# Kernel optimization log

Hardware: AMD Instinct MI355X
Metric: run time of the kernel (lower is better)

Reference implementation:

```python
import jax, jax.numpy as jnp
import numpy as np
from jax import lax

ALPHA = 2.0   # snntorch surrogate.atan(alpha=2.0)
THR = 1.0     # snntorch Leaky default threshold
NUM_STEPS = 8

@jax.custom_vjp
def spike(x):
    # Heaviside forward, ATan surrogate backward (matches snntorch surrogate.atan)
    return (x > 0).astype(x.dtype)

def _spk_fwd(x):
    return (x > 0).astype(x.dtype), x

def _spk_bwd(x, g):
    return (g * (ALPHA / 2.0) / (1.0 + (jnp.pi / 2.0 * ALPHA * x) ** 2),)

spike.defvjp(_spk_fwd, _spk_bwd)


def setup_inputs() -> dict:
    key = jax.random.key(0)
    ks = jax.random.split(key, 7)
    B, D, H, A = 16384, 512, 2048, 8
    H2 = H // 2
    s1 = 1.0 / np.sqrt(D)
    s2 = 1.0 / np.sqrt(H)
    s3 = 1.0 / np.sqrt(H2)
    return {
        "x": jax.random.normal(ks[0], (B, D), jnp.float32),
        "W1": jax.random.uniform(ks[1], (H, D), jnp.float32, -s1, s1),
        "b1": jax.random.uniform(ks[2], (H,), jnp.float32, -s1, s1),
        "W2": jax.random.uniform(ks[3], (H2, H), jnp.float32, -s2, s2),
        "b2": jax.random.uniform(ks[4], (H2,), jnp.float32, -s2, s2),
        "Wo": jax.random.uniform(ks[5], (A, H2), jnp.float32, -s3, s3),
        "bo": jax.random.uniform(ks[6], (A,), jnp.float32, -s3, s3),
        "beta1": jnp.float32(0.9),
        "beta2": jnp.float32(0.85),
        "beta_out": jnp.float32(0.95),
    }


def reference(x, W1, b1, W2, b2, Wo, bo, beta1, beta2, beta_out):
    B = x.shape[0]
    H, H2, A = W1.shape[0], W2.shape[0], Wo.shape[0]
    # snntorch clamps learnable beta into [0, 1] inside the state function
    be1 = jnp.clip(beta1, 0.0, 1.0)
    be2 = jnp.clip(beta2, 0.0, 1.0)
    beo = jnp.clip(beta_out, 0.0, 1.0)

    cur1 = x @ W1.T + b1  # fc1(x) is identical every step; hoist out of the loop

    mem1 = jnp.zeros((B, H), x.dtype)
    mem2 = jnp.zeros((B, H2), x.dtype)
    mem_out = jnp.zeros((B, A), x.dtype)
    max_mem = jnp.full((B, A), -1e9, x.dtype)

    def step(carry, _):
        mem1, mem2, mem_out, max_mem = carry
        # lif1: subtract-reset Leaky; reset uses detached spike of previous mem
        reset1 = lax.stop_gradient(spike(mem1 - THR))
        mem1 = be1 * mem1 + cur1 - reset1 * THR
        spk1 = spike(mem1 - THR)
        # lif2
        reset2 = lax.stop_gradient(spike(mem2 - THR))
        mem2 = be2 * mem2 + (spk1 @ W2.T + b2) - reset2 * THR
        spk2 = spike(mem2 - THR)
        # li_out: reset_mechanism='none' -> pure leaky integrator
        mem_out = beo * mem_out + (spk2 @ Wo.T + bo)
        max_mem = jnp.maximum(max_mem, mem_out)
        return (mem1, mem2, mem_out, max_mem), None

    (mem1, mem2, mem_out, max_mem), _ = lax.scan(
        step, (mem1, mem2, mem_out, max_mem), None, length=NUM_STEPS
    )
    return max_mem
```

## Files before the change

kernel.cpp:

```cpp
#include <hip/hip_runtime.h>
#include <stdint.h>


typedef __bf16 bf16;
typedef __attribute__((ext_vector_type(8))) __bf16 bf16x8;
typedef __attribute__((ext_vector_type(4))) float f32x4;

#define CAP1 2097152
#define CAP2 2097152
#define MARGIN 2e-3f
#define MARGIN2 5e-4f

__device__ __forceinline__ void gl16(const void* g, void* l) {
  __builtin_amdgcn_global_load_lds(
      (const __attribute__((address_space(1))) uint32_t*)g,
      (__attribute__((address_space(3))) uint32_t*)l, 16, 0, 0);
}

__device__ __forceinline__ float clampf(float v) {
  return fminf(fmaxf(v, 0.f), 1.f);
}

__device__ __forceinline__ uint32_t expand2(uint32_t b) {
  return ((b & 1u) ? 0x3F80u : 0u) | ((b & 2u) ? 0x3F800000u : 0u);
}


__global__ void split_x_kernel(const float* __restrict__ x, bf16* __restrict__ Ax) {
  int i = blockIdx.x * 256 + threadIdx.x;
  int b = i >> 9, d = i & 511;
  float v = x[i];
  bf16 hi = (bf16)v;
  bf16 lo = (bf16)(v - (float)hi);
  size_t base = (size_t)b * 1024;
  Ax[base + d] = hi;
  Ax[base + 512 + d] = lo;
}

__global__ void split_w1_kernel(const float* __restrict__ W1, bf16* __restrict__ B0,
                                bf16* __restrict__ B1) {
  int i = blockIdx.x * 256 + threadIdx.x;
  int r = i >> 9, d = i & 511;
  float v = W1[i];
  bf16 hi = (bf16)v;
  bf16 lo = (bf16)(v - (float)hi);
  size_t base = (size_t)r * 1024;
  B0[base + d] = hi;  B0[base + 512 + d] = lo;
  B1[base + d] = lo;  B1[base + 512 + d] = hi;
}

__global__ void split_w2_kernel(const float* __restrict__ W2, bf16* __restrict__ Wh,
                                bf16* __restrict__ Wl) {
  int i = blockIdx.x * 256 + threadIdx.x;
  float v = W2[i];
  bf16 hi = (bf16)v;
  Wh[i] = hi;
  Wl[i] = (bf16)(v - (float)hi);
}


#define SA_OFF  0
#define SB0_OFF 16384
#define SB1_OFF 32768

__global__ __launch_bounds__(256, 2) void gemm1_lif1_kernel(
    const bf16* __restrict__ A, const bf16* __restrict__ B0,
    const bf16* __restrict__ B1, const float* __restrict__ bias,
    const float* __restrict__ beta1p,
    uint32_t* __restrict__ spkbits1, uint2* __restrict__ flag1,
    uint32_t* __restrict__ cnt1)
{
  __shared__ __align__(16) uint8_t lds[49152];
  const int tid = threadIdx.x;
  const int lane = tid & 63;
  const int wave = tid >> 6;
  const int wm = (wave >> 1) * 64, wn = (wave & 1) * 64;
  const size_t brow = (size_t)blockIdx.x * 128;
  const size_t bcol = (size_t)blockIdx.y * 128;
  const int K = 1024;
  const float be = clampf(beta1p[0]);

  const bf16* gA  = A  + brow * K;
  const bf16* gB0 = B0 + bcol * K;
  const bf16* gB1 = B1 + bcol * K;

  f32x4 acc[4][4] = {};

  for (int kk = 0; kk < K; kk += 64) {
#pragma unroll
    for (int q = 0; q < 4; ++q) {
      const int flat = q * 256 + tid;
      const int row = flat >> 3;
      const int s   = flat & 7;
      const int c8  = (s ^ (row & 7)) * 8;
      gl16(gA  + (size_t)row * K + kk + c8, lds + SA_OFF  + flat * 16);
      gl16(gB0 + (size_t)row * K + kk + c8, lds + SB0_OFF + flat * 16);
      gl16(gB1 + (size_t)row * K + kk + c8, lds + SB1_OFF + flat * 16);
    }
    asm volatile("s_waitcnt vmcnt(0)" ::: "memory");
    __syncthreads();
#pragma unroll
    for (int ks = 0; ks < 2; ++ks) {
      bf16x8 af[4], b0f[4], b1f[4];
#pragma unroll
      for (int i = 0; i < 4; ++i) {
        const int ra = wm + i * 16 + (lane & 15);
        const int sa = ((ks * 4 + (lane >> 4)) ^ (ra & 7)) * 16;
        af[i]  = *(const bf16x8*)(lds + SA_OFF  + ra * 128 + sa);
        const int rb = wn + i * 16 + (lane & 15);
        const int sb = ((ks * 4 + (lane >> 4)) ^ (rb & 7)) * 16;
        b0f[i] = *(const bf16x8*)(lds + SB0_OFF + rb * 128 + sb);
        b1f[i] = *(const bf16x8*)(lds + SB1_OFF + rb * 128 + sb);
      }
#pragma unroll
      for (int m = 0; m < 4; ++m)
#pragma unroll
        for (int n = 0; n < 4; ++n) {
          acc[m][n] = __builtin_amdgcn_mfma_f32_16x16x32_bf16(af[m], b0f[n], acc[m][n], 0, 0, 0);
          acc[m][n] = __builtin_amdgcn_mfma_f32_16x16x32_bf16(af[m], b1f[n], acc[m][n], 0, 0, 0);
        }
    }
    __syncthreads();
  }

  uint32_t* lcnt  = (uint32_t*)lds;
  uint32_t* lbase = (uint32_t*)(lds + 4);
  uint2*    llist = (uint2*)(lds + 16);
  const uint32_t CAPL = 3000;
  if (tid == 0) *lcnt = 0;
  __syncthreads();

  const int rg = lane >> 4;
  const bool writer = (lane & 15) == 0;
  uint16_t* sp16 = (uint16_t*)spkbits1;

#pragma unroll
  for (int m = 0; m < 4; ++m)
#pragma unroll
    for (int n = 0; n < 4; ++n) {
      const int chb = (int)(bcol) + wn + n * 16;
      const int w32 = chb >> 5, half = (chb >> 4) & 1;
      const float bv = bias[chb + (lane & 15)];
#pragma unroll
      for (int j = 0; j < 4; ++j) {
        const float c = acc[m][n][j] + bv;
        float mem = 0.f; uint32_t hist = 0; bool nearThr = false;
#pragma unroll
        for (int t = 0; t < 8; ++t) {
          float rst = (mem > 1.f) ? 1.f : 0.f;
          mem = be * mem + c - rst;
          uint32_t bit = (mem > 1.f) ? 1u : 0u;
          hist |= bit << t;
          nearThr |= (fabsf(mem - 1.f) < MARGIN);
        }
#pragma unroll
        for (int t = 0; t < 8; ++t) {
          unsigned long long bal = __ballot((hist >> t) & 1u);
          if (writer) {
            uint32_t row = (uint32_t)(brow + wm + m * 16 + rg * 4 + j);
            size_t idx = ((size_t)(t * 64 + w32) * 16384 + row) * 2 + half;
            sp16[idx] = (uint16_t)(bal >> (rg * 16));
          }
        }
        if (nearThr) {
          const uint32_t h = (uint32_t)(chb + (lane & 15));
          const uint32_t b = (uint32_t)(brow + wm + m * 16 + rg * 4 + j);
          uint2 en; en.x = (h << 14) | b; en.y = hist;
          uint32_t pos = atomicAdd(lcnt, 1u);
          if (pos < CAPL) llist[pos] = en;
          else { uint32_t g = atomicAdd(cnt1, 1u); if (g < CAP1) flag1[g] = en; }
        }
      }
    }

  __syncthreads();
  uint32_t ln = *lcnt; if (ln > CAPL) ln = CAPL;
  if (tid == 0) *lbase = atomicAdd(cnt1, ln);
  __syncthreads();
  const uint32_t gb = *lbase;
  for (uint32_t i = tid; i < ln; i += 256) {
    uint32_t g = gb + i;
    if (g < CAP1) flag1[g] = llist[i];
  }
}


__global__ __launch_bounds__(256) void repair1_kernel(
    const float* __restrict__ x, const float* __restrict__ W1,
    const float* __restrict__ b1, const float* __restrict__ beta1p,
    const uint2* __restrict__ flag1, const uint32_t* __restrict__ cnt1,
    uint32_t* __restrict__ spkbits1)
{
  uint32_t n = cnt1[0]; if (n > CAP1) n = CAP1;
  const float be = clampf(beta1p[0]);
  for (uint32_t i = blockIdx.x * 256 + threadIdx.x; i < n; i += gridDim.x * 256) {
    uint2 e = flag1[i];
    int h = e.x >> 14, b = e.x & 16383;
    const float* xr = x + (size_t)b * 512;
    const float* wr = W1 + (size_t)h * 512;
    float s = 0.f;
    for (int d = 0; d < 512; ++d) s = fmaf(xr[d], wr[d], s);
    s = __fadd_rn(s, b1[h]);
    float m = 0.f; uint32_t eb = 0;
#pragma unroll
    for (int t = 0; t < 8; ++t) {
      float rst = (__fsub_rn(m, 1.f) > 0.f) ? 1.f : 0.f;
      m = __fsub_rn(__fadd_rn(__fmul_rn(be, m), s), rst);
      if (__fsub_rn(m, 1.f) > 0.f) eb |= 1u << t;
    }
    uint32_t diff = eb ^ (e.y & 0xFFu);
    if (diff) {
#pragma unroll
      for (int t = 0; t < 8; ++t)
        if ((diff >> t) & 1u)
          atomicXor(&spkbits1[((size_t)t * 64 + (h >> 5)) * 16384 + b], 1u << (h & 31));
    }
  }
}


__global__ __launch_bounds__(256, 2) void step2_kernel(
    const uint32_t* __restrict__ spkbits1,
    const bf16* __restrict__ W2h, const bf16* __restrict__ W2l,
    const float* __restrict__ b2, const float* __restrict__ beta2p,
    uint32_t* __restrict__ spkbits2, uint32_t* __restrict__ flag2,
    uint32_t* __restrict__ cnt2)
{
  __shared__ __align__(16) uint8_t lds[49152];
  const int K = 2048;
  const int tid = threadIdx.x;
  const int lane = tid & 63;
  const int wave = tid >> 6;
  const int wm = (wave >> 1) * 64, wn = (wave & 1) * 64;
  const size_t brow = (size_t)blockIdx.x * 128;
  const size_t bcol = (size_t)blockIdx.y * 128;
  const float be2 = clampf(beta2p[0]);

  const bf16* gB0 = W2h + bcol * K;
  const bf16* gB1 = W2l + bcol * K;

  float b2c[4];
#pragma unroll
  for (int n = 0; n < 4; ++n) b2c[n] = b2[bcol + wn + n * 16 + (lane & 15)];

  const int ar = tid & 127;
  const int aw = tid >> 7;
  const int rg = lane >> 4;
  const bool writer = (lane & 15) == 0;
  uint16_t* sp16 = (uint16_t*)spkbits2;

  f32x4 acc[4][4] = {};
  unsigned long long flg = 0;

  for (int t = 0; t < 8; ++t) {
#pragma unroll
    for (int m = 0; m < 4; ++m)
#pragma unroll
      for (int n = 0; n < 4; ++n)
#pragma unroll
        for (int j = 0; j < 4; ++j) {
          float v = acc[m][n][j];
          float rst = (v > 1.f) ? 1.f : 0.f;
          acc[m][n][j] = be2 * v + (b2c[n] - rst);
        }

    for (int kk = 0; kk < K; kk += 64) {
      uint32_t bits = spkbits1[((size_t)t * 64 + (kk >> 5) + aw) * 16384 + brow + ar];
#pragma unroll
      for (int c = 0; c < 4; ++c) {
        uint4 u;
        u.x = expand2(bits >> (8 * c));
        u.y = expand2(bits >> (8 * c + 2));
        u.z = expand2(bits >> (8 * c + 4));
        u.w = expand2(bits >> (8 * c + 6));
        const int slot = (aw * 4 + c) ^ (ar & 7);
        *(uint4*)(lds + SA_OFF + ar * 128 + slot * 16) = u;
      }
#pragma unroll
      for (int q = 0; q < 4; ++q) {
        const int flat = q * 256 + tid;
        const int row = flat >> 3;
        const int s   = flat & 7;
        const int c8  = (s ^ (row & 7)) * 8;
        gl16(gB0 + (size_t)row * K + kk + c8, lds + SB0_OFF + flat * 16);
        gl16(gB1 + (size_t)row * K + kk + c8, lds + SB1_OFF + flat * 16);
      }
      asm volatile("s_waitcnt vmcnt(0)" ::: "memory");
      __syncthreads();
#pragma unroll
      for (int ks = 0; ks < 2; ++ks) {
        bf16x8 af[4], b0f[4], b1f[4];
#pragma unroll
        for (int i = 0; i < 4; ++i) {
          const int ra = wm + i * 16 + (lane & 15);
          const int sa = ((ks * 4 + (lane >> 4)) ^ (ra & 7)) * 16;
          af[i] = *(const bf16x8*)(lds + SA_OFF + ra * 128 + sa);
          const int rb = wn + i * 16 + (lane & 15);
          const int sb = ((ks * 4 + (lane >> 4)) ^ (rb & 7)) * 16;
          b0f[i] = *(const bf16x8*)(lds + SB0_OFF + rb * 128 + sb);
          b1f[i] = *(const bf16x8*)(lds + SB1_OFF + rb * 128 + sb);
        }
#pragma unroll
        for (int m = 0; m < 4; ++m)
#pragma unroll
          for (int n = 0; n < 4; ++n) {
            acc[m][n] = __builtin_amdgcn_mfma_f32_16x16x32_bf16(af[m], b0f[n], acc[m][n], 0, 0, 0);
            acc[m][n] = __builtin_amdgcn_mfma_f32_16x16x32_bf16(af[m], b1f[n], acc[m][n], 0, 0, 0);
          }
      }
      __syncthreads();
    }

#pragma unroll
    for (int m = 0; m < 4; ++m)
#pragma unroll
      for (int n = 0; n < 4; ++n) {
        const int chb = (int)(bcol) + wn + n * 16;
        const int w32 = chb >> 5, half = (chb >> 4) & 1;
#pragma unroll
        for (int j = 0; j < 4; ++j) {
          float v = acc[m][n][j];
          if (fabsf(v - 1.f) < MARGIN2) flg |= 1ull << (m * 16 + n * 4 + j);
          unsigned long long bal = __ballot(v > 1.f);
          if (writer) {
            uint32_t row = (uint32_t)(brow + wm + m * 16 + rg * 4 + j);
            size_t idx = ((size_t)(t * 32 + w32) * 16384 + row) * 2 + half;
            sp16[idx] = (uint16_t)(bal >> (rg * 16));
          }
        }
      }
  }

  uint32_t* lcnt  = (uint32_t*)lds;
  uint32_t* lbase = (uint32_t*)(lds + 4);
  uint32_t* llist = (uint32_t*)(lds + 16);
  const uint32_t CAPL = 6000;
  if (tid == 0) *lcnt = 0;
  __syncthreads();

  if (flg) {
#pragma unroll
    for (int m = 0; m < 4; ++m)
#pragma unroll
      for (int n = 0; n < 4; ++n)
#pragma unroll
        for (int j = 0; j < 4; ++j)
          if ((flg >> (m * 16 + n * 4 + j)) & 1ull) {
            const int row = wm + m * 16 + rg * 4 + j;
            const int col = wn + n * 16 + (lane & 15);
            uint32_t en = (uint32_t)(((brow + row) << 10) | (bcol + col));
            uint32_t pos = atomicAdd(lcnt, 1u);
            if (pos < CAPL) llist[pos] = en;
            else { uint32_t g = atomicAdd(cnt2, 1u); if (g < CAP2) flag2[g] = en; }
          }
  }

  __syncthreads();
  uint32_t ln = *lcnt; if (ln > CAPL) ln = CAPL;
  if (tid == 0) *lbase = atomicAdd(cnt2, ln);
  __syncthreads();
  const uint32_t gb = *lbase;
  for (uint32_t i = tid; i < ln; i += 256) {
    uint32_t g = gb + i;
    if (g < CAP2) flag2[g] = llist[i];
  }
}


__global__ __launch_bounds__(256) void repair2_kernel(
    const uint32_t* __restrict__ spkbits1, const float* __restrict__ W2,
    const float* __restrict__ b2, const float* __restrict__ beta2p,
    const uint32_t* __restrict__ flag2, const uint32_t* __restrict__ cnt2,
    uint32_t* __restrict__ spkbits2)
{
  uint32_t n = cnt2[0]; if (n > CAP2) n = CAP2;
  const float be = clampf(beta2p[0]);
  for (uint32_t i = blockIdx.x * 256 + threadIdx.x; i < n; i += gridDim.x * 256) {
    uint32_t e = flag2[i];
    int b = e >> 10, h2 = e & 1023;
    const float* wr = W2 + (size_t)h2 * 2048;
    const float bias = b2[h2];
    float s[8] = {0, 0, 0, 0, 0, 0, 0, 0};
    for (int w = 0; w < 64; ++w) {
      uint32_t bt[8];
#pragma unroll
      for (int t = 0; t < 8; ++t)
        bt[t] = spkbits1[((size_t)t * 64 + w) * 16384 + b];
#pragma unroll 8
      for (int k = 0; k < 32; ++k) {
        const float wv = wr[w * 32 + k];
#pragma unroll
        for (int t = 0; t < 8; ++t) {
          float addend = ((bt[t] >> k) & 1u) ? wv : 0.0f;
          s[t] = __fadd_rn(s[t], addend);
        }
      }
    }
    float m = 0.f;
#pragma unroll
    for (int t = 0; t < 8; ++t) {
      float st = __fadd_rn(s[t], bias);
      float rst = (__fsub_rn(m, 1.f) > 0.f) ? 1.f : 0.f;
      m = __fsub_rn(__fadd_rn(__fmul_rn(be, m), st), rst);
      uint32_t exact = (__fsub_rn(m, 1.f) > 0.f) ? 1u : 0u;
      uint32_t* wp = &spkbits2[((size_t)t * 32 + (h2 >> 5)) * 16384 + b];
      uint32_t stored = (*wp >> (h2 & 31)) & 1u;
      if (stored != exact) atomicXor(wp, 1u << (h2 & 31));
    }
  }
}


__global__ __launch_bounds__(256) void out_kernel(
    const uint32_t* __restrict__ spkbits2, const float* __restrict__ Wo,
    const float* __restrict__ bo, const float* __restrict__ betaop,
    float* __restrict__ out)
{
  const int wave = threadIdx.x >> 6, lane = threadIdx.x & 63;
  const int b = blockIdx.x * 4 + wave;
  const float beo = clampf(betaop[0]);
  const int a = lane & 7;
  const int slice = lane >> 3;

  float s[8] = {0, 0, 0, 0, 0, 0, 0, 0};
#pragma unroll
  for (int q = 0; q < 4; ++q) {
    const int wrd = slice * 4 + q;
    uint32_t wt[8];
#pragma unroll
    for (int t = 0; t < 8; ++t)
      wt[t] = spkbits2[((size_t)(t * 32 + wrd)) * 16384 + b];
    const float* wop = Wo + (size_t)a * 1024 + wrd * 32;
#pragma unroll
    for (int k8 = 0; k8 < 8; ++k8) {
      const float4 wv = *(const float4*)(wop + k8 * 4);
      const float wa[4] = {wv.x, wv.y, wv.z, wv.w};
#pragma unroll
      for (int kk = 0; kk < 4; ++kk) {
        const int k = k8 * 4 + kk;
#pragma unroll
        for (int t = 0; t < 8; ++t)
          s[t] += ((wt[t] >> k) & 1u) ? wa[kk] : 0.0f;
      }
    }
  }
#pragma unroll
  for (int t = 0; t < 8; ++t) {
    s[t] += __shfl_down(s[t], 8, 64);
    s[t] += __shfl_down(s[t], 16, 64);
    s[t] += __shfl_down(s[t], 32, 64);
  }
  if (lane < 8) {
    const float bov = bo[a];
    float mo = 0.f, mx = -1e30f;
#pragma unroll
    for (int t = 0; t < 8; ++t) {
      mo = beo * mo + (s[t] + bov);
      mx = fmaxf(mx, mo);
    }
    out[(size_t)b * 8 + a] = mx;
  }
}

__global__ void zero_hdr_kernel(uint32_t* p) {
  if (threadIdx.x < 64) p[threadIdx.x] = 0;
}

__global__ void fill_sentinel(float* out, int n, float v) {
  int i = blockIdx.x * 256 + threadIdx.x;
  if (i < n) out[i] = v;
}


extern "C" void kernel_launch(void* const* d_in, const int* in_sizes, int n_in,
                              void* d_out, int out_size, void* d_ws, size_t ws_size,
                              hipStream_t stream)
{
  (void)in_sizes; (void)n_in;
  const float* x   = (const float*)d_in[0];
  const float* W1  = (const float*)d_in[1];
  const float* b1  = (const float*)d_in[2];
  const float* W2  = (const float*)d_in[3];
  const float* b2  = (const float*)d_in[4];
  const float* Wo  = (const float*)d_in[5];
  const float* bo  = (const float*)d_in[6];
  const float* be1 = (const float*)d_in[7];
  const float* be2 = (const float*)d_in[8];
  const float* beo = (const float*)d_in[9];
  float* out = (float*)d_out;

  const int B = 16384, D = 512, H = 2048, H2 = 1024;

  const size_t sz_hdr  = 256;
  const size_t sz_Ax   = (size_t)B * 1024 * 2;
  const size_t sz_W1s  = (size_t)H * 1024 * 2;
  const size_t sz_W2s  = (size_t)H2 * H * 2;
  const size_t sz_b1   = (size_t)8 * 64 * B * 4;
  const size_t sz_b2   = (size_t)8 * 32 * B * 4;
  const size_t sz_f1   = (size_t)CAP1 * 8;
  const size_t sz_f2   = (size_t)CAP2 * 4;
  const size_t need = sz_hdr + sz_Ax + 2 * sz_W1s + 2 * sz_W2s +
                      sz_b1 + sz_b2 + sz_f1 + sz_f2;

  if (ws_size < need) {
    fill_sentinel<<<(out_size + 255) / 256, 256, 0, stream>>>(
        out, out_size, 1000.0f + (float)(ws_size >> 20));
    return;
  }

  uint8_t* p = (uint8_t*)d_ws;
  uint32_t* hdr = (uint32_t*)p;     p += sz_hdr;
  bf16* Ax      = (bf16*)p;         p += sz_Ax;
  bf16* W1B0    = (bf16*)p;         p += sz_W1s;
  bf16* W1B1    = (bf16*)p;         p += sz_W1s;
  bf16* W2h     = (bf16*)p;         p += sz_W2s;
  bf16* W2l     = (bf16*)p;         p += sz_W2s;
  uint32_t* spkbits1 = (uint32_t*)p; p += sz_b1;
  uint32_t* spkbits2 = (uint32_t*)p; p += sz_b2;
  uint2* flag1  = (uint2*)p;        p += sz_f1;
  uint32_t* flag2 = (uint32_t*)p;   p += sz_f2;
  uint32_t* cnt1 = hdr + 0;
  uint32_t* cnt2 = hdr + 1;

  zero_hdr_kernel<<<1, 64, 0, stream>>>(hdr);
  split_x_kernel <<<(B * D) / 256, 256, 0, stream>>>(x, Ax);
  split_w1_kernel<<<(H * D) / 256, 256, 0, stream>>>(W1, W1B0, W1B1);
  split_w2_kernel<<<(H2 * H) / 256, 256, 0, stream>>>(W2, W2h, W2l);

  gemm1_lif1_kernel<<<dim3(B / 128, H / 128), 256, 0, stream>>>(
      Ax, W1B0, W1B1, b1, be1, spkbits1, flag1, cnt1);
  repair1_kernel<<<256, 256, 0, stream>>>(x, W1, b1, be1, flag1, cnt1, spkbits1);

  step2_kernel<<<dim3(B / 128, H2 / 128), 256, 0, stream>>>(
      spkbits1, W2h, W2l, b2, be2, spkbits2, flag2, cnt2);
  repair2_kernel<<<256, 256, 0, stream>>>(spkbits1, W2, b2, be2, flag2, cnt2, spkbits2);

  out_kernel<<<B / 4, 256, 0, stream>>>(spkbits2, Wo, bo, beo, out);
}
```

Measured before the change: 1.803 ms.

## Double-buffer W2 tiles and expand spike bits in registers in step2

Reworks the step2 GEMM loop so the W2 hi/lo tiles are double-buffered in LDS. The next k-tile's global-to-LDS loads are issued before the current tile's MFMAs, with a partial vmcnt wait replacing the full drain. The spike-bit A operand is no longer expanded into LDS: each lane loads its packed words straight from global memory and expands them into bf16 fragments in registers, which removes the A-side LDS writes and reads. The cost is 64KB of LDS per block, which may limit the two-blocks-per-CU occupancy, plus more live registers and fragile hand-set wait counts.

```diff
diff --git a/kernel.cpp b/kernel.cpp
--- a/kernel.cpp
+++ b/kernel.cpp
@@ -219,6 +219,8 @@
 }
 
 
+#define BOFF(d) ((d) * 32768)
+
 __global__ __launch_bounds__(256, 2) void step2_kernel(
     const uint32_t* __restrict__ spkbits1,
     const bf16* __restrict__ W2h, const bf16* __restrict__ W2l,
@@ -226,7 +228,7 @@
     uint32_t* __restrict__ spkbits2, uint32_t* __restrict__ flag2,
     uint32_t* __restrict__ cnt2)
 {
-  __shared__ __align__(16) uint8_t lds[49152];
+  __shared__ __align__(16) uint8_t lds[65536];
   const int K = 2048;
   const int tid = threadIdx.x;
   const int lane = tid & 63;
@@ -243,14 +245,87 @@
 #pragma unroll
   for (int n = 0; n < 4; ++n) b2c[n] = b2[bcol + wn + n * 16 + (lane & 15)];
 
-  const int ar = tid & 127;
-  const int aw = tid >> 7;
   const int rg = lane >> 4;
-  const bool writer = (lane & 15) == 0;
+  const int lnlo = lane & 15;
+  const int sh8 = rg * 8;
+  const bool writer = lnlo == 0;
   uint16_t* sp16 = (uint16_t*)spkbits2;
+
+  const int sflat = tid * 4;
+  (void)sflat;
 
   f32x4 acc[4][4] = {};
   unsigned long long flg = 0;
+
+#define STAGE_B(D, KKN)                                                       \
+  {                                                                           \
+    _Pragma("unroll")                                                         \
+    for (int q = 0; q < 4; ++q) {                                             \
+      const int flat = q * 256 + tid;                                         \
+      const int row = flat >> 3;                                              \
+      const int s = flat & 7;                                                 \
+      const int c8 = (s ^ (row & 7)) * 8;                                     \
+      gl16(gB0 + (size_t)row * K + (KKN) * 64 + c8, lds + BOFF(D) + flat * 16);\
+      gl16(gB1 + (size_t)row * K + (KKN) * 64 + c8,                           \
+           lds + BOFF(D) + 16384 + flat * 16);                                \
+    }                                                                         \
+  }
+
+#define LOAD_A(AW, TT, KKN)                                                   \
+  {                                                                           \
+    const uint32_t* pA =                                                      \
+        spkbits1 + ((size_t)((TT) * 64 + (KKN) * 2)) * 16384 + brow;          \
+    _Pragma("unroll")                                                         \
+    for (int ks = 0; ks < 2; ++ks)                                            \
+      _Pragma("unroll")                                                       \
+      for (int i = 0; i < 4; ++i)                                             \
+        AW[ks][i] = pA[(size_t)ks * 16384 + wm + i * 16 + lnlo];              \
+  }
+
+#define COMPUTE(AW, D)                                                        \
+  {                                                                           \
+    bf16x8 af[2][4];                                                          \
+    _Pragma("unroll")                                                         \
+    for (int ks = 0; ks < 2; ++ks)                                            \
+      _Pragma("unroll")                                                       \
+      for (int i = 0; i < 4; ++i) {                                           \
+        uint32_t byte = (AW[ks][i] >> sh8) & 0xFFu;                           \
+        uint4 u;                                                              \
+        u.x = expand2(byte);                                                  \
+        u.y = expand2(byte >> 2);                                             \
+        u.z = expand2(byte >> 4);                                             \
+        u.w = expand2(byte >> 6);                                             \
+        af[ks][i] = *(bf16x8*)&u;                                             \
+      }                                                                       \
+    asm volatile("s_waitcnt vmcnt(16)" ::: "memory");                         \
+    __builtin_amdgcn_s_barrier();                                             \
+    _Pragma("unroll")                                                         \
+    for (int ks = 0; ks < 2; ++ks) {                                          \
+      bf16x8 b0f[4], b1f[4];                                                  \
+      _Pragma("unroll")                                                       \
+      for (int i = 0; i < 4; ++i) {                                           \
+        const int rb = wn + i * 16 + lnlo;                                    \
+        const int sb = ((ks * 4 + rg) ^ (rb & 7)) * 16;                       \
+        b0f[i] = *(const bf16x8*)(lds + BOFF(D) + rb * 128 + sb);             \
+        b1f[i] = *(const bf16x8*)(lds + BOFF(D) + 16384 + rb * 128 + sb);     \
+      }                                                                       \
+      _Pragma("unroll")                                                       \
+      for (int m = 0; m < 4; ++m)                                             \
+        _Pragma("unroll")                                                     \
+        for (int n = 0; n < 4; ++n) {                                         \
+          acc[m][n] = __builtin_amdgcn_mfma_f32_16x16x32_bf16(                \
+              af[ks][m], b0f[n], acc[m][n], 0, 0, 0);                         \
+          acc[m][n] = __builtin_amdgcn_mfma_f32_16x16x32_bf16(                \
+              af[ks][m], b1f[n], acc[m][n], 0, 0, 0);                         \
+        }                                                                     \
+    }                                                                         \
+    __builtin_amdgcn_s_barrier();                                             \
+  }
+
+  uint32_t awA[2][4], awB[2][4];
+
+  LOAD_A(awA, 0, 0);
+  STAGE_B(0, 0);
 
   for (int t = 0; t < 8; ++t) {
 #pragma unroll
@@ -264,51 +339,21 @@
           acc[m][n][j] = be2 * v + (b2c[n] - rst);
         }
 
-    for (int kk = 0; kk < K; kk += 64) {
-      uint32_t bits = spkbits1[((size_t)t * 64 + (kk >> 5) + aw) * 16384 + brow + ar];
-#pragma unroll
-      for (int c = 0; c < 4; ++c) {
-        uint4 u;
-        u.x = expand2(bits >> (8 * c));
-        u.y = expand2(bits >> (8 * c + 2));
-        u.z = expand2(bits >> (8 * c + 4));
-        u.w = expand2(bits >> (8 * c + 6));
-        const int slot = (aw * 4 + c) ^ (ar & 7);
-        *(uint4*)(lds + SA_OFF + ar * 128 + slot * 16) = u;
-      }
-#pragma unroll
-      for (int q = 0; q < 4; ++q) {
-        const int flat = q * 256 + tid;
-        const int row = flat >> 3;
-        const int s   = flat & 7;
-        const int c8  = (s ^ (row & 7)) * 8;
-        gl16(gB0 + (size_t)row * K + kk + c8, lds + SB0_OFF + flat * 16);
-        gl16(gB1 + (size_t)row * K + kk + c8, lds + SB1_OFF + flat * 16);
-      }
-      asm volatile("s_waitcnt vmcnt(0)" ::: "memory");
-      __syncthreads();
-#pragma unroll
-      for (int ks = 0; ks < 2; ++ks) {
-        bf16x8 af[4], b0f[4], b1f[4];
-#pragma unroll
-        for (int i = 0; i < 4; ++i) {
-          const int ra = wm + i * 16 + (lane & 15);
-          const int sa = ((ks * 4 + (lane >> 4)) ^ (ra & 7)) * 16;
-          af[i] = *(const bf16x8*)(lds + SA_OFF + ra * 128 + sa);
-          const int rb = wn + i * 16 + (lane & 15);
-          const int sb = ((ks * 4 + (lane >> 4)) ^ (rb & 7)) * 16;
-          b0f[i] = *(const bf16x8*)(lds + SB0_OFF + rb * 128 + sb);
-          b1f[i] = *(const bf16x8*)(lds + SB1_OFF + rb * 128 + sb);
-        }
-#pragma unroll
-        for (int m = 0; m < 4; ++m)
-#pragma unroll
-          for (int n = 0; n < 4; ++n) {
-            acc[m][n] = __builtin_amdgcn_mfma_f32_16x16x32_bf16(af[m], b0f[n], acc[m][n], 0, 0, 0);
-            acc[m][n] = __builtin_amdgcn_mfma_f32_16x16x32_bf16(af[m], b1f[n], acc[m][n], 0, 0, 0);
-          }
-      }
-      __syncthreads();
+#pragma unroll
+    for (int kk2 = 0; kk2 < 16; ++kk2) {
+      {
+        const int nk = 2 * kk2 + 1;
+        LOAD_A(awB, t, nk);
+        STAGE_B(1, nk);
+        COMPUTE(awA, 0);
+      }
+      {
+        const int nk = (2 * kk2 + 2) & 31;
+        const int nt = (kk2 == 15) ? ((t < 7) ? t + 1 : 7) : t;
+        LOAD_A(awA, nt, nk);
+        STAGE_B(0, nk);
+        COMPUTE(awB, 1);
+      }
     }
 
 #pragma unroll
@@ -331,6 +376,7 @@
       }
   }
 
+  __syncthreads();
   uint32_t* lcnt  = (uint32_t*)lds;
   uint32_t* lbase = (uint32_t*)(lds + 4);
   uint32_t* llist = (uint32_t*)(lds + 16);
@@ -347,7 +393,7 @@
         for (int j = 0; j < 4; ++j)
           if ((flg >> (m * 16 + n * 4 + j)) & 1ull) {
             const int row = wm + m * 16 + rg * 4 + j;
-            const int col = wn + n * 16 + (lane & 15);
+            const int col = wn + n * 16 + lnlo;
             uint32_t en = (uint32_t)(((brow + row) << 10) | (bcol + col));
             uint32_t pos = atomicAdd(lcnt, 1u);
             if (pos < CAPL) llist[pos] = en;
@@ -364,6 +410,9 @@
     uint32_t g = gb + i;
     if (g < CAP2) flag2[g] = llist[i];
   }
+#undef STAGE_B
+#undef LOAD_A
+#undef COMPUTE
 }
 
 
```

Result: slower. 3.654 ms (+102.7%).
